# Kernel optimization log

Hardware: AMD Instinct MI355X
Metric: run time of the kernel (lower is better)

## Reference

```python
import jax, jax.numpy as jnp
import numpy as np

N_EMB = 4096
EMB_DIM = 256
BETA = 0.25


def setup_inputs() -> dict:
    key = jax.random.key(0)
    k1, k2 = jax.random.split(key)
    z = jax.random.normal(k1, (32, EMB_DIM, 32, 32), dtype=jnp.float32)
    # nn.Embedding weight initialized uniform(-1/n_emb, 1/n_emb)
    embedding = jax.random.uniform(
        k2, (N_EMB, EMB_DIM), dtype=jnp.float32,
        minval=-1.0 / N_EMB, maxval=1.0 / N_EMB)
    return {"z": z, "embedding": embedding}


def reference(z, embedding):
    sg = jax.lax.stop_gradient
    # (B,C,H,W) -> (B,H,W,C)
    zp = jnp.transpose(z, (0, 2, 3, 1))
    zf = zp.reshape(-1, EMB_DIM)  # [N, D]
    # squared distances: ||z||^2 + ||e||^2 - 2 z e^T  -> [N, n_emb]
    d = (jnp.sum(zf * zf, axis=1, keepdims=True)
         + jnp.sum(embedding * embedding, axis=1)
         - 2.0 * jnp.matmul(zf, embedding.T))
    idx = jnp.argmin(d, axis=1)  # [N]
    min_encodings = jax.nn.one_hot(idx, N_EMB, dtype=zf.dtype)  # [N, n_emb]
    e_mean = jnp.mean(min_encodings, axis=0)
    perplexity = jnp.exp(-jnp.sum(e_mean * jnp.log(e_mean + 1e-10)))
    # gather codebook rows (same math as one-hot matmul)
    z_q = jnp.take(embedding, idx, axis=0).reshape(zp.shape)
    # straight-through estimator
    z_q_st = zp + sg(z_q - zp)
    q_latent_loss = jnp.mean((z_q_st - sg(zp)) ** 2)
    e_latent_loss = jnp.mean((sg(z_q_st) - zp) ** 2)
    loss = q_latent_loss + BETA * e_latent_loss
    z_q_out = jnp.transpose(z_q_st, (0, 3, 1, 2))  # (B,C,H,W)
    return (loss, z_q_out, perplexity, min_encodings, idx[:, None])
```

## Files before the change

kernel.cpp:

```cpp
#include <hip/hip_runtime.h>

#define N_ROWS 32768
#define NEMB   4096
#define DIM    256

#define O_LOSS 0
#define O_ZQ   1ull
#define O_PERP 8388609ull
#define O_ENC  8388610ull
#define O_IDX  142606338ull
#define Z4_BEG 2097153
#define Z4_END 35651584

#define CAP    32
#define EPS    1e-3f

typedef unsigned long long u64;
typedef __attribute__((ext_vector_type(8))) __bf16 bf16x8;
typedef __attribute__((ext_vector_type(4))) float  f32x4;


__device__ __forceinline__ unsigned int f2bf1(float x) {
    unsigned int u = __float_as_uint(x);
    return (u + 0x7fffu + ((u >> 16) & 1u)) >> 16;
}
__device__ __forceinline__ unsigned int f2bf2(float lo, float hi) {
    return f2bf1(lo) | (f2bf1(hi) << 16);
}

__global__ __launch_bounds__(256)
void vq_prep(const float* __restrict__ emb, unsigned short* __restrict__ embsw,
             int* __restrict__ counts, float* __restrict__ out)
{
    const int tid = threadIdx.x, blk = blockIdx.x;
    const int base = (blk << 8) + tid;
#pragma unroll
    for (int q = 0; q < 4; ++q) {
        const int ch = (base << 2) + q;
        const int code = ch >> 5, cw = ch & 31;
        const float* ep = emb + (size_t)code * 256 + cw * 8;
        float4 e0 = *(const float4*)ep;
        float4 e1 = *(const float4*)(ep + 4);
        uint4 pk = make_uint4(f2bf2(e0.x, e0.y), f2bf2(e0.z, e0.w),
                              f2bf2(e1.x, e1.y), f2bf2(e1.z, e1.w));
        *(uint4*)((char*)embsw + (size_t)code * 512 + (size_t)((cw ^ (code & 7)) << 4)) = pk;
    }
    if (blk == 0) {
        for (int j = tid; j < NEMB; j += 256) counts[j] = 0;
        if (tid == 0) {
            out[O_ENC] = 0.f; out[O_ENC + 1] = 0.f;
            out[(size_t)Z4_END * 4] = 0.f; out[(size_t)Z4_END * 4 + 1] = 0.f;
        }
    }
}

__global__ __launch_bounds__(512, 2)
void vq_filter(const float* __restrict__ z, const float* __restrict__ emb,
               const unsigned short* __restrict__ embsw,
               float* __restrict__ out, u64* __restrict__ ws_best)
{
#pragma clang fp contract(off)
    __shared__ __align__(16) char Bsh[65536];
    __shared__ float zsumS[256];
    __shared__ float rowmaxS[256];
    __shared__ unsigned short rowlist[256][CAP];
    __shared__ int rowcnt[256];
    __shared__ int nflag;
    __shared__ int flagrows[32];
    __shared__ u64 flagbest[32];

    const int tid = threadIdx.x;
    const int blk = blockIdx.x;
    const int rb  = blk >> 1;
    const int hv  = blk & 1;
    const int n0  = rb << 8;
    const int C0  = hv << 11;
    const int b   = n0 >> 10;
    const int hw0 = n0 & 1023;
    const int w    = tid >> 6;
    const int lane = tid & 63;
    const int r0w  = w << 5;
    const int arow = lane & 15;
    const int akg  = lane >> 4;
    const float* zb = z + (size_t)b * 262144 + hw0;

    if (tid < 32) flagbest[tid] = ~0ull;
    if (tid == 0) nflag = 0;

    if (tid < 256) {
        rowcnt[tid] = 0;
        const float* gz = zb + tid;
        float hs0, hs1;
        {
            float r[8];
#pragma unroll
            for (int j = 0; j < 8; ++j) { float v = gz[(size_t)j << 10]; r[j] = v * v; }
            for (int m = 1; m < 16; ++m)
#pragma unroll
                for (int j = 0; j < 8; ++j) {
                    float v = gz[(size_t)(8 * m + j) << 10];
                    float sq = v * v;
                    r[j] = r[j] + sq;
                }
            hs0 = ((r[0] + r[1]) + (r[2] + r[3])) + ((r[4] + r[5]) + (r[6] + r[7]));
        }
        {
            float r[8];
#pragma unroll
            for (int j = 0; j < 8; ++j) { float v = gz[(size_t)(128 + j) << 10]; r[j] = v * v; }
            for (int m = 1; m < 16; ++m)
#pragma unroll
                for (int j = 0; j < 8; ++j) {
                    float v = gz[(size_t)(128 + 8 * m + j) << 10];
                    float sq = v * v;
                    r[j] = r[j] + sq;
                }
            hs1 = ((r[0] + r[1]) + (r[2] + r[3])) + ((r[4] + r[5]) + (r[6] + r[7]));
        }
        zsumS[tid] = hs0 + hs1;
    }

    bf16x8 A[2][8];
#pragma unroll
    for (int rf = 0; rf < 2; ++rf) {
        const float* zr = zb + r0w + rf * 16 + arow;
#pragma unroll
        for (int s = 0; s < 8; ++s) {
            union { unsigned int u[4]; bf16x8 v; } cvt;
#pragma unroll
            for (int p = 0; p < 4; ++p) {
                const int c = s * 32 + akg * 8 + 2 * p;
                const float lo = zr[(size_t)c << 10];
                const float hi = zr[(size_t)(c + 1) << 10];
                cvt.u[p] = f2bf2(lo, hi);
            }
            A[rf][s] = cvt.v;
        }
    }

    auto stage = [&](int buf, int ct) {
        const char* sb = (const char*)embsw + (((size_t)(C0 + (ct << 6))) << 9)
                         + (w << 10) + (lane << 4);
        char* db = Bsh + buf * 32768 + (w << 10);
#pragma unroll
        for (int it = 0; it < 4; ++it) {
            __builtin_amdgcn_global_load_lds(
                (const __attribute__((address_space(1))) unsigned int*)(sb + it * 8192),
                (__attribute__((address_space(3))) unsigned int*)(db + it * 8192),
                16, 0, 0);
        }
    };

    float vmax[2][4];
#pragma unroll
    for (int rf = 0; rf < 2; ++rf)
#pragma unroll
        for (int j = 0; j < 4; ++j) vmax[rf][j] = -3.4e38f;
    float thr[2][4];

    const size_t zf_base = (size_t)Z4_BEG + (size_t)blk * 131072;

    for (int pass = 0; pass < 2; ++pass) {
        stage(0, 0);
        __syncthreads();
        for (int ct = 0; ct < 32; ++ct) {
            const int buf = ct & 1;
            if (ct < 31) stage(buf ^ 1, ct + 1);

            {
                const int iter = pass * 32 + ct;
                const size_t g = zf_base + (size_t)iter * 2048 + tid;
                const float4 zv = make_float4(0.f, 0.f, 0.f, 0.f);
#pragma unroll
                for (int q = 0; q < 4; ++q) {
                    const size_t i4 = g + (size_t)q * 512;
                    if (i4 < (size_t)Z4_END) ((float4*)out)[i4] = zv;
                }
            }

            f32x4 acc[2][4];
            const f32x4 zz = {0.f, 0.f, 0.f, 0.f};
#pragma unroll
            for (int rf = 0; rf < 2; ++rf)
#pragma unroll
                for (int cf = 0; cf < 4; ++cf) acc[rf][cf] = zz;

            const char* bufp = Bsh + buf * 32768;
#pragma unroll
            for (int s = 0; s < 8; ++s) {
#pragma unroll
                for (int cf = 0; cf < 4; ++cf) {
                    const int cl = (cf << 4) + arow;
                    const int off = (cl << 9) + (((s << 6) + (akg << 4)) ^ ((cl & 7) << 4));
                    bf16x8 bb = *(const bf16x8*)(bufp + off);
                    acc[0][cf] = __builtin_amdgcn_mfma_f32_16x16x32_bf16(A[0][s], bb, acc[0][cf], 0, 0, 0);
                    acc[1][cf] = __builtin_amdgcn_mfma_f32_16x16x32_bf16(A[1][s], bb, acc[1][cf], 0, 0, 0);
                }
            }

            if (pass == 0) {
#pragma unroll
                for (int rf = 0; rf < 2; ++rf)
#pragma unroll
                    for (int cf = 0; cf < 4; ++cf)
#pragma unroll
                        for (int j = 0; j < 4; ++j)
                            vmax[rf][j] = fmaxf(vmax[rf][j], acc[rf][cf][j]);
            } else {
#pragma unroll
                for (int rf = 0; rf < 2; ++rf)
#pragma unroll
                    for (int cf = 0; cf < 4; ++cf)
#pragma unroll
                        for (int j = 0; j < 4; ++j) {
                            const float v = acc[rf][cf][j];
                            if (v >= thr[rf][j]) {
                                const int row  = r0w + rf * 16 + akg * 4 + j;
                                const int code = (ct << 6) + (cf << 4) + arow;
                                const int slot = atomicAdd(&rowcnt[row], 1);
                                if (slot < CAP) rowlist[row][slot] = (unsigned short)code;
                                else if (slot == CAP) {
                                    const int fi = atomicAdd(&nflag, 1);
                                    if (fi < 32) flagrows[fi] = row;
                                }
                            }
                        }
            }
            __syncthreads();
        }
        if (pass == 0) {
#pragma unroll
            for (int rf = 0; rf < 2; ++rf)
#pragma unroll
                for (int j = 0; j < 4; ++j) {
                    float v = vmax[rf][j];
                    v = fmaxf(v, __shfl_xor(v, 1));
                    v = fmaxf(v, __shfl_xor(v, 2));
                    v = fmaxf(v, __shfl_xor(v, 4));
                    v = fmaxf(v, __shfl_xor(v, 8));
                    vmax[rf][j] = v;
                }
            if ((lane & 15) == 0) {
#pragma unroll
                for (int rf = 0; rf < 2; ++rf)
#pragma unroll
                    for (int j = 0; j < 4; ++j)
                        rowmaxS[r0w + rf * 16 + akg * 4 + j] = vmax[rf][j];
            }
            __syncthreads();
#pragma unroll
            for (int rf = 0; rf < 2; ++rf)
#pragma unroll
                for (int j = 0; j < 4; ++j)
                    thr[rf][j] = rowmaxS[r0w + rf * 16 + akg * 4 + j] - EPS;
        }
    }
    __syncthreads();

    if (tid < 256) {
        const int cnt = rowcnt[tid];
        if (cnt <= CAP) {
            const float zs = zsumS[tid];
            const float* zrow = zb + tid;
            u64 bestk = ~0ull;
            for (int basec = 0; basec < cnt; basec += 8) {
                int codes[8];
#pragma unroll
                for (int j = 0; j < 8; ++j) {
                    const int jj = basec + j;
                    codes[j] = rowlist[tid][jj < cnt ? jj : basec];
                }
                const float* ep[8];
#pragma unroll
                for (int j = 0; j < 8; ++j) ep[j] = emb + ((size_t)(C0 + codes[j]) << 8);
                float a8[8] = {0.f, 0.f, 0.f, 0.f, 0.f, 0.f, 0.f, 0.f};
#pragma unroll 2
                for (int k4 = 0; k4 < 64; ++k4) {
                    const float zv0 = zrow[(size_t)(4 * k4 + 0) << 10];
                    const float zv1 = zrow[(size_t)(4 * k4 + 1) << 10];
                    const float zv2 = zrow[(size_t)(4 * k4 + 2) << 10];
                    const float zv3 = zrow[(size_t)(4 * k4 + 3) << 10];
                    float4 e4[8];
#pragma unroll
                    for (int j = 0; j < 8; ++j) e4[j] = *(const float4*)(ep[j] + 4 * k4);
#pragma unroll
                    for (int j = 0; j < 8; ++j) {
                        a8[j] = fmaf(zv0, e4[j].x, a8[j]);
                        a8[j] = fmaf(zv1, e4[j].y, a8[j]);
                        a8[j] = fmaf(zv2, e4[j].z, a8[j]);
                        a8[j] = fmaf(zv3, e4[j].w, a8[j]);
                    }
                }
#pragma unroll
                for (int j = 0; j < 8; ++j) {
                    if (basec + j < cnt) {
                        const float d = fmaf(-2.f, a8[j], zs);
                        const u64 key = ((u64)__float_as_uint(d) << 32)
                                      | (unsigned)(C0 + codes[j]);
                        if (key < bestk) bestk = key;
                    }
                }
            }
            ws_best[((size_t)(n0 + tid) << 1) + hv] = bestk;
        }
    }
    __syncthreads();

    const int nf = (nflag > 32) ? 32 : nflag;
    for (int f = 0; f < nf; ++f) {
        const int fr = flagrows[f];
        if (tid < 256) {
            const float zs = zsumS[fr];
            const float* zrow = zb + fr;
            const float* ep0 = emb + ((size_t)(C0 + (tid << 3)) << 8);
            float a8[8] = {0.f, 0.f, 0.f, 0.f, 0.f, 0.f, 0.f, 0.f};
#pragma unroll 2
            for (int k4 = 0; k4 < 64; ++k4) {
                const float zv0 = zrow[(size_t)(4 * k4 + 0) << 10];
                const float zv1 = zrow[(size_t)(4 * k4 + 1) << 10];
                const float zv2 = zrow[(size_t)(4 * k4 + 2) << 10];
                const float zv3 = zrow[(size_t)(4 * k4 + 3) << 10];
#pragma unroll
                for (int j = 0; j < 8; ++j) {
                    const float4 e4 = *(const float4*)(ep0 + (size_t)j * 256 + 4 * k4);
                    a8[j] = fmaf(zv0, e4.x, a8[j]);
                    a8[j] = fmaf(zv1, e4.y, a8[j]);
                    a8[j] = fmaf(zv2, e4.z, a8[j]);
                    a8[j] = fmaf(zv3, e4.w, a8[j]);
                }
            }
            u64 bk = ~0ull;
#pragma unroll
            for (int j = 0; j < 8; ++j) {
                const float d = fmaf(-2.f, a8[j], zs);
                const u64 key = ((u64)__float_as_uint(d) << 32)
                              | (unsigned)(C0 + (tid << 3) + j);
                if (key < bk) bk = key;
            }
            atomicMin(&flagbest[f], bk);
        }
    }
    __syncthreads();
    if (tid < nf) ws_best[((size_t)(n0 + flagrows[tid]) << 1) + hv] = flagbest[tid];
}

__global__ __launch_bounds__(256)
void vq_zq(const float* __restrict__ z, const float* __restrict__ emb,
           const u64* __restrict__ ws_best, float* __restrict__ out,
           int* __restrict__ counts, double* __restrict__ parts)
{
#pragma clang fp contract(off)
    __shared__ float embT[32][257];
    __shared__ int idxS[32];
    __shared__ double red[256];

    const int tid = threadIdx.x;
    const int blk = blockIdx.x;
    const int b   = blk >> 5;
    const int hw0 = (blk & 31) << 5;
    const int n0  = (b << 10) + hw0;

    if (tid < 32) {
        const int n = n0 + tid;
        u64 m = ws_best[(size_t)n * 2];
        u64 v = ws_best[(size_t)n * 2 + 1];
        if (v < m) m = v;
        const int id = (int)(m & 0xffffffffu);
        idxS[tid] = id;
        out[O_IDX + n] = (float)id;
        out[O_ENC + (size_t)n * 4096 + id] = 1.0f;
        atomicAdd(&counts[id], 1);
    }
    __syncthreads();

    {
        const int g = tid >> 3, l8 = tid & 7;
        const float* er = emb + (size_t)idxS[g] * 256;
#pragma unroll
        for (int it = 0; it < 8; ++it) {
            const float4 v = *(const float4*)(er + it * 32 + l8 * 4);
            const int c = it * 32 + l8 * 4;
            embT[g][c]     = v.x;
            embT[g][c + 1] = v.y;
            embT[g][c + 2] = v.z;
            embT[g][c + 3] = v.w;
        }
    }
    __syncthreads();

    const int r  = tid & 31;
    const int cq = tid >> 5;
    const size_t base = (size_t)b * 262144 + hw0 + r;
    double val = 0.0;
#pragma unroll 4
    for (int i = 0; i < 32; ++i) {
        const int c = i * 8 + cq;
        const size_t gid = base + (size_t)c * 1024;
        const float zp = z[gid];
        const float e  = embT[r][c];
        const float t  = e - zp;
        const float zq = zp + t;
        __builtin_nontemporal_store(zq, &out[O_ZQ + gid]);
        const float diff = zq - zp;
        val += (double)(diff * diff);
    }

    red[tid] = val;
    __syncthreads();
    for (int st = 128; st > 0; st >>= 1) {
        if (tid < st) red[tid] += red[tid + st];
        __syncthreads();
    }
    if (tid == 0) parts[blk] = red[0];
}

__global__ void vq_final(const int* __restrict__ counts,
                         const double* __restrict__ parts, float* __restrict__ out)
{
    __shared__ double red[256];
    const int t = threadIdx.x;

    double loc = 0.0;
    for (int j = t; j < NEMB; j += 256) {
        float em = (float)counts[j] * (1.0f / 32768.0f);
        float lt = em + 1e-10f;
        float lg = logf(lt);
        float pr = em * lg;
        loc += (double)pr;
    }
    red[t] = loc;
    __syncthreads();
    for (int st = 128; st > 0; st >>= 1) {
        if (t < st) red[t] += red[t + st];
        __syncthreads();
    }
    double s = red[0];
    __syncthreads();

    double q = 0.0;
    for (int j = t; j < 1024; j += 256) q += parts[j];
    red[t] = q;
    __syncthreads();
    for (int st = 128; st > 0; st >>= 1) {
        if (t < st) red[t] += red[t + st];
        __syncthreads();
    }
    if (t == 0) {
        out[O_PERP] = expf(-(float)s);
        double qm = red[0] * (1.0 / 8388608.0);
        float  qf = (float)qm;
        out[O_LOSS] = qf + 0.25f * qf;
    }
}

extern "C" void kernel_launch(void* const* d_in, const int* in_sizes, int n_in,
                              void* d_out, int out_size, void* d_ws, size_t ws_size,
                              hipStream_t stream)
{
    const float* z   = (const float*)d_in[0];
    const float* emb = (const float*)d_in[1];
    float* out = (float*)d_out;

    u64*    ws_best = (u64*)d_ws;
    int*    counts  = (int*)((char*)d_ws + 1048576);
    double* parts   = (double*)((char*)d_ws + 1064960);

    unsigned short* embsw = (unsigned short*)((char*)d_out + 16 + 16777216);

    vq_prep   <<<128,  256, 0, stream>>>(emb, embsw, counts, out);
    vq_filter <<<256,  512, 0, stream>>>(z, emb, embsw, out, ws_best);
    vq_zq     <<<1024, 256, 0, stream>>>(z, emb, ws_best, out, counts, parts);
    vq_final  <<<1,    256, 0, stream>>>(counts, parts, out);
}
```

Measured before the change: 935.1 us.

## Move one-hot encoding zero-fill from filter kernel into zq kernel

The zeroing of the large one-hot encodings buffer moves out of the MFMA distance/filter kernel, where it was interleaved with the compute loop. It now runs in the per-row zq kernel, where each block clears its own 32 rows of 4096 floats before writing the 1.0 entries. The z_q stores also switch from nontemporal to regular stores. This takes store bandwidth off the compute-bound filter kernel at the cost of a larger, purely store-bound zq kernel, so the two no longer overlap compute and memory traffic.

```diff
diff --git a/kernel.cpp b/kernel.cpp
--- a/kernel.cpp
+++ b/kernel.cpp
@@ -9,8 +9,6 @@
 #define O_PERP 8388609ull
 #define O_ENC  8388610ull
 #define O_IDX  142606338ull
-#define Z4_BEG 2097153
-#define Z4_END 35651584
 
 #define CAP    32
 #define EPS    1e-3f
@@ -30,7 +28,7 @@
 
 __global__ __launch_bounds__(256)
 void vq_prep(const float* __restrict__ emb, unsigned short* __restrict__ embsw,
-             int* __restrict__ counts, float* __restrict__ out)
+             int* __restrict__ counts)
 {
     const int tid = threadIdx.x, blk = blockIdx.x;
     const int base = (blk << 8) + tid;
@@ -47,17 +45,13 @@
     }
     if (blk == 0) {
         for (int j = tid; j < NEMB; j += 256) counts[j] = 0;
-        if (tid == 0) {
-            out[O_ENC] = 0.f; out[O_ENC + 1] = 0.f;
-            out[(size_t)Z4_END * 4] = 0.f; out[(size_t)Z4_END * 4 + 1] = 0.f;
-        }
     }
 }
 
 __global__ __launch_bounds__(512, 2)
 void vq_filter(const float* __restrict__ z, const float* __restrict__ emb,
                const unsigned short* __restrict__ embsw,
-               float* __restrict__ out, u64* __restrict__ ws_best)
+               u64* __restrict__ ws_best)
 {
 #pragma clang fp contract(off)
     __shared__ __align__(16) char Bsh[65536];
@@ -158,25 +152,12 @@
         for (int j = 0; j < 4; ++j) vmax[rf][j] = -3.4e38f;
     float thr[2][4];
 
-    const size_t zf_base = (size_t)Z4_BEG + (size_t)blk * 131072;
-
     for (int pass = 0; pass < 2; ++pass) {
         stage(0, 0);
         __syncthreads();
         for (int ct = 0; ct < 32; ++ct) {
             const int buf = ct & 1;
             if (ct < 31) stage(buf ^ 1, ct + 1);
-
-            {
-                const int iter = pass * 32 + ct;
-                const size_t g = zf_base + (size_t)iter * 2048 + tid;
-                const float4 zv = make_float4(0.f, 0.f, 0.f, 0.f);
-#pragma unroll
-                for (int q = 0; q < 4; ++q) {
-                    const size_t i4 = g + (size_t)q * 512;
-                    if (i4 < (size_t)Z4_END) ((float4*)out)[i4] = zv;
-                }
-            }
 
             f32x4 acc[2][4];
             const f32x4 zz = {0.f, 0.f, 0.f, 0.f};
@@ -368,10 +349,25 @@
         const int id = (int)(m & 0xffffffffu);
         idxS[tid] = id;
         out[O_IDX + n] = (float)id;
-        out[O_ENC + (size_t)n * 4096 + id] = 1.0f;
         atomicAdd(&counts[id], 1);
     }
-    __syncthreads();
+
+    {
+        const size_t S  = (size_t)O_ENC + (size_t)n0 * 4096;
+        const size_t q4 = (S + 2) >> 2;
+        const float4 zv = make_float4(0.f, 0.f, 0.f, 0.f);
+#pragma unroll
+        for (int i = 0; i < 128; ++i) {
+            const size_t i4 = q4 + tid + ((size_t)i << 8);
+            if (i4 < q4 + 32767) ((float4*)out)[i4] = zv;
+        }
+        if (tid == 0) { out[S] = 0.f; out[S + 1] = 0.f; }
+        if (tid == 1) { out[S + 131070] = 0.f; out[S + 131071] = 0.f; }
+    }
+    __syncthreads();
+
+    if (tid < 32)
+        out[(size_t)O_ENC + (size_t)(n0 + tid) * 4096 + idxS[tid]] = 1.0f;
 
     {
         const int g = tid >> 3, l8 = tid & 7;
@@ -400,7 +396,7 @@
         const float e  = embT[r][c];
         const float t  = e - zp;
         const float zq = zp + t;
-        __builtin_nontemporal_store(zq, &out[O_ZQ + gid]);
+        out[O_ZQ + gid] = zq;
         const float diff = zq - zp;
         val += (double)(diff * diff);
     }
@@ -467,8 +463,8 @@
 
     unsigned short* embsw = (unsigned short*)((char*)d_out + 16 + 16777216);
 
-    vq_prep   <<<128,  256, 0, stream>>>(emb, embsw, counts, out);
-    vq_filter <<<256,  512, 0, stream>>>(z, emb, embsw, out, ws_best);
+    vq_prep   <<<128,  256, 0, stream>>>(emb, embsw, counts);
+    vq_filter <<<256,  512, 0, stream>>>(z, emb, embsw, ws_best);
     vq_zq     <<<1024, 256, 0, stream>>>(z, emb, ws_best, out, counts, parts);
     vq_final  <<<1,    256, 0, stream>>>(counts, parts, out);
 }
```

Measured after the change: 1.004 ms. 1.07x slower.
